# Performance work log

Measured on AMD Instinct MI355X. Metric: run time of the kernel, lower is better.

Reference implementation:

```python
import jax, jax.numpy as jnp
import numpy as np

N, D, HID, G, E2 = 2048, 256, 128, 8, 16384


def _mlp(h, w1, b1, g, be, w2, b2):
    # Linear -> ReLU -> BatchNorm1d (training mode, biased batch var) -> Linear
    h = jax.nn.relu(h @ w1 + b1)
    mu = h.mean(axis=0)
    var = ((h - mu) ** 2).mean(axis=0)
    h = (h - mu) / jnp.sqrt(var + 1e-5) * g + be
    return h @ w2 + b2


def setup_inputs() -> dict:
    key = jax.random.key(0)
    ks = jax.random.split(key, 12)
    x = jax.random.normal(ks[0], (N, D), jnp.float32)
    src = jax.random.randint(ks[1], (E2,), 0, N)
    dst = jax.random.randint(ks[2], (E2,), 0, N)
    src = jnp.where(src == dst, (src + 1) % N, src)  # no self loops
    edge_index = jnp.stack([jnp.concatenate([src, dst]),
                            jnp.concatenate([dst, src])])  # symmetric
    batch = jnp.sort(jax.random.randint(ks[3], (N,), 0, G))
    def lin(k, i, o):
        return 0.1 * jax.random.normal(k, (i, o), jnp.float32)
    out = dict(x=x, edge_index=edge_index, batch=batch)
    dims = [(1, HID, HID), (HID, HID, HID), (HID, HID, 1)]
    names = [("w11", "b11", "g1", "be1", "w12", "b12"),
             ("w21", "b21", "g2", "be2", "w22", "b22"),
             ("w31", "b31", "g3", "be3", "w32", "b32")]
    k = 4
    for (i, h, o), n in zip(dims, names):
        out[n[0]] = lin(ks[k], i, h)
        out[n[1]] = jnp.zeros((h,), jnp.float32)
        out[n[2]] = jnp.ones((h,), jnp.float32)
        out[n[3]] = jnp.zeros((h,), jnp.float32)
        out[n[4]] = lin(ks[k + 1], h, o)
        out[n[5]] = jnp.zeros((o,), jnp.float32)
        k += 2
    return out


def reference(x, edge_index, batch,
              w11, b11, g1, be1, w12, b12,
              w21, b21, g2, be2, w22, b22,
              w31, b31, g3, be3, w32, b32):
    n = x.shape[0]
    # dense adjacency from edge_index; L = D - A (unnormalized graph Laplacian)
    A = jnp.zeros((n, n), x.dtype).at[edge_index[0], edge_index[1]].set(1.0)
    deg = A.sum(axis=1)
    # entropy term: V = x*(Lx) - x*(Ax) + A(x*x), Lx = deg*x - Ax
    Ax = A @ x
    V = x * (deg[:, None] * x - Ax) - x * Ax + A @ (x * x)
    V = jnp.linalg.norm(V, axis=1)  # [n]
    # per-graph softmax over the batch segments
    mx = jax.ops.segment_max(V, batch, num_segments=G)
    ex = jnp.exp(V - mx[batch])
    P = ex / jax.ops.segment_sum(ex, batch, num_segments=G)[batch]
    P = jnp.where(P == 0.0, 1.0, P)
    ent = -P * jnp.log(P)  # [n]

    # GINConv (eps=0): mlp(x + sum_{j in N(i)} x_j) = mlp(x + A @ x)
    def gin(h, w1, b1, g, be, w2, b2):
        return _mlp(h + A @ h, w1, b1, g, be, w2, b2)

    h = gin(ent[:, None], w11, b11, g1, be1, w12, b12)
    h = gin(h, w21, b21, g2, be2, w22, b22)
    h = gin(h, w31, b31, g3, be3, w32, b32)
    p = jax.nn.sigmoid(h[:, 0])  # [n] node probabilities

    gamma = ent.sum()
    loss = gamma - jnp.vdot(ent, p) + jnp.vdot(p, A @ p)

    # greedy conditional expectation (sequential MIS-style selection)
    order = jnp.argsort(-p)

    def step(carry, idx):
        dummy, sel, rej = carry
        nb = A[idx] > 0.0  # neighbor mask [n]
        deg0 = ~jnp.any(nb)
        sel = sel.at[idx].set(sel[idx] | deg0)  # isolated node -> selected
        eligible = (~rej[idx]) & (~sel[idx])
        s = jnp.where(nb, 0.0, dummy).at[idx].set(1.0)
        li = gamma - jnp.vdot(ent, s) + jnp.vdot(s, A @ s)
        accept = eligible & (li <= loss)
        sel = sel.at[idx].set(sel[idx] | accept)
        rej = rej | (nb & accept)
        dummy = jnp.where(accept, s, dummy)
        return (dummy, sel, rej), None

    init = (p, jnp.zeros(n, dtype=bool), jnp.zeros(n, dtype=bool))
    (dummy, sel, rej), _ = jax.lax.scan(step, init, order)

    # graph reconstruction (masked instead of compacted, for static shapes)
    mask = sel.astype(x.dtype)
    x_pooled = x * mask[:, None]
    A2 = A @ A
    A3 = A2 @ A
    eye = jnp.eye(n, dtype=x.dtype)
    adj_pooled = (1.0 - eye) * jnp.clip(A2 + A3, 0.0, 1.0) * (mask[:, None] * mask[None, :])
    batch_pooled = jnp.where(sel, batch, -1)
    return x_pooled, adj_pooled, sel, batch_pooled, loss
```

## Files before the change

### kernel.cpp

```cpp
#include <hip/hip_runtime.h>
#include <math.h>

#define NN 2048
#define DIMF 256
#define HIDN 128
#define NG 8
#define NEDGES 32768
#define W32 32
#define TRI_CAP 131072
#define TRI_LDS 4864

typedef unsigned long long u64;
typedef unsigned char u8;
typedef unsigned short u16;

__global__ void k_init(u64* __restrict__ rowbits, int* __restrict__ segstart) {
  int i = blockIdx.x * blockDim.x + threadIdx.x;
  for (int k = i; k < NN * W32; k += gridDim.x * blockDim.x) rowbits[k] = 0ull;
  if (i <= NG) segstart[i] = NN;
}

__global__ void k_edges(const int* __restrict__ ei, u64* __restrict__ rowbits) {
  int e = blockIdx.x * blockDim.x + threadIdx.x;
  if (e >= NEDGES) return;
  int u = ei[e], v = ei[NEDGES + e];
  atomicOr(&rowbits[((size_t)u << 5) + (v >> 6)], 1ull << (v & 63));
}

__global__ void k_deg(const u64* __restrict__ rowbits, int* __restrict__ deg,
                      const int* __restrict__ batch, int* __restrict__ segstart) {
  int i = blockIdx.x * blockDim.x + threadIdx.x;
  if (i >= NN) return;
  int c = 0;
  for (int w = 0; w < W32; ++w) c += __popcll(rowbits[(i << 5) + w]);
  deg[i] = c;
  if (i == 0 || batch[i] != batch[i - 1]) segstart[batch[i]] = i;
}

__global__ void k_scan2048(const int* __restrict__ in, int* __restrict__ out) {
  __shared__ int part[256];
  int t = threadIdx.x;
  int v[8]; int s = 0;
  for (int k = 0; k < 8; ++k) { v[k] = in[t * 8 + k]; s += v[k]; }
  part[t] = s;
  __syncthreads();
  for (int off = 1; off < 256; off <<= 1) {
    int y = (t >= off) ? part[t - off] : 0;
    __syncthreads();
    part[t] += y;
    __syncthreads();
  }
  int run = part[t] - s;
  for (int k = 0; k < 8; ++k) { out[t * 8 + k] = run; run += v[k]; }
  if (t == 255) out[NN] = part[255];
}

__global__ void k_extract(const u64* __restrict__ rowbits, const int* __restrict__ rp,
                          int* __restrict__ col, int* __restrict__ cnt) {
  int i = blockIdx.x * blockDim.x + threadIdx.x;
  if (i >= NN) return;
  const u64* ri = rowbits + ((size_t)i << 5);
  int o = rp[i];
  for (int w = 0; w < W32; ++w) {
    u64 b = ri[w];
    while (b) { col[o++] = (w << 6) + __builtin_ctzll(b); b &= b - 1; }
  }
  int c = 0;
  for (int e = rp[i]; e < o; ++e) {
    const u64* ra = rowbits + ((size_t)col[e] << 5);
    for (int w = 0; w < W32; ++w) c += __popcll(ra[w] & ri[w]);
  }
  cnt[i] = c;
}

__global__ void k_trifill(const u64* __restrict__ rowbits, const int* __restrict__ rp,
                          const int* __restrict__ col, const int* __restrict__ tp,
                          int2* __restrict__ tri) {
  int i = blockIdx.x * blockDim.x + threadIdx.x;
  if (i >= NN) return;
  const u64* ri = rowbits + ((size_t)i << 5);
  int o = tp[i];
  for (int e = rp[i]; e < rp[i + 1]; ++e) {
    int a = col[e];
    const u64* ra = rowbits + ((size_t)a << 5);
    for (int w = 0; w < W32; ++w) {
      u64 b = ra[w] & ri[w];
      while (b) {
        int j = (w << 6) + __builtin_ctzll(b);
        if (o < TRI_CAP) tri[o] = make_int2(a, j);
        ++o;
        b &= b - 1;
      }
    }
  }
}

__global__ void k_V(const float* __restrict__ x, const int* __restrict__ rp,
                    const int* __restrict__ col, float* __restrict__ V) {
  int i = blockIdx.x; int t = threadIdx.x;
  float xi = x[i * DIMF + t];
  float s1 = 0.f, s2 = 0.f;
  int r0 = rp[i], r1 = rp[i + 1];
  for (int e = r0; e < r1; ++e) {
    float xj = x[col[e] * DIMF + t];
    s1 += xj; s2 += xj * xj;
  }
  float dg = (float)(r1 - r0);
  float val = dg * xi * xi - 2.f * xi * s1 + s2;
  __shared__ double red[DIMF];
  red[t] = (double)val * (double)val;
  __syncthreads();
  for (int off = DIMF / 2; off > 0; off >>= 1) { if (t < off) red[t] += red[t + off]; __syncthreads(); }
  if (t == 0) V[i] = (float)sqrt(red[0]);
}

__global__ void k_soft(const float* __restrict__ V, const int* __restrict__ segstart,
                       float* __restrict__ ent, double* __restrict__ seggamma) {
  int g = blockIdx.x; int t = threadIdx.x;
  int s = segstart[g];
  int e = NN;
  for (int gg = g + 1; gg <= NG; ++gg) { int v = segstart[gg]; if (v < e) e = v; }
  if (s >= e) { if (t == 0) seggamma[g] = 0.0; return; }
  __shared__ float fm[256];
  __shared__ double dd[256];
  float m = -3.0e38f;
  for (int i = s + t; i < e; i += 256) m = fmaxf(m, V[i]);
  fm[t] = m; __syncthreads();
  for (int off = 128; off > 0; off >>= 1) { if (t < off) fm[t] = fmaxf(fm[t], fm[t + off]); __syncthreads(); }
  float mx = fm[0];
  __syncthreads();
  double sum = 0.0;
  for (int i = s + t; i < e; i += 256) sum += exp((double)V[i] - (double)mx);
  dd[t] = sum; __syncthreads();
  for (int off = 128; off > 0; off >>= 1) { if (t < off) dd[t] += dd[t + off]; __syncthreads(); }
  double tot = dd[0];
  __syncthreads();
  double gs = 0.0;
  for (int i = s + t; i < e; i += 256) {
    double P = exp((double)V[i] - (double)mx) / tot;
    float ev = (P > 0.0) ? (float)(-P * log(P)) : 0.f;
    ent[i] = ev;
    gs += (double)ev;
  }
  dd[t] = gs; __syncthreads();
  for (int off = 128; off > 0; off >>= 1) { if (t < off) dd[t] += dd[t + off]; __syncthreads(); }
  if (t == 0) seggamma[g] = dd[0];
}

__global__ void k_agg1(const float* __restrict__ ent, const int* __restrict__ rp,
                       const int* __restrict__ col, float* __restrict__ agg) {
  int i = blockIdx.x * blockDim.x + threadIdx.x;
  if (i >= NN) return;
  float a = ent[i];
  for (int e = rp[i]; e < rp[i + 1]; ++e) a += ent[col[e]];
  agg[i] = a;
}

__global__ void k_lin1(const float* __restrict__ agg, const float* __restrict__ w,
                       const float* __restrict__ b, float* __restrict__ t) {
  int idx = blockIdx.x * blockDim.x + threadIdx.x;
  if (idx >= NN * HIDN) return;
  int i = idx >> 7, k = idx & 127;
  float v = agg[i] * w[k] + b[k];
  t[idx] = v > 0.f ? v : 0.f;
}

__global__ void k_bn(const float* __restrict__ t, const float* __restrict__ g,
                     const float* __restrict__ be, float* __restrict__ scale,
                     float* __restrict__ shift) {
  int k = blockIdx.x; int tid = threadIdx.x;
  __shared__ double red[256];
  double s = 0.0;
  for (int i = tid; i < NN; i += 256) s += (double)t[i * HIDN + k];
  red[tid] = s; __syncthreads();
  for (int off = 128; off > 0; off >>= 1) { if (tid < off) red[tid] += red[tid + off]; __syncthreads(); }
  double mu = red[0] / NN;
  __syncthreads();
  double v = 0.0;
  for (int i = tid; i < NN; i += 256) { double dv = (double)t[i * HIDN + k] - mu; v += dv * dv; }
  red[tid] = v; __syncthreads();
  for (int off = 128; off > 0; off >>= 1) { if (tid < off) red[tid] += red[tid + off]; __syncthreads(); }
  if (tid == 0) {
    float var = (float)(red[0] / NN);
    float sc = g[k] / sqrtf(var + 1e-5f);
    scale[k] = sc;
    shift[k] = be[k] - (float)mu * sc;
  }
}

template<int PRE, int RELU>
__global__ void k_mm(const float* __restrict__ in, const float* __restrict__ Wm,
                     const float* __restrict__ bias, const float* __restrict__ scale,
                     const float* __restrict__ shift, float* __restrict__ out) {
  __shared__ float ti[8][HIDN];
  int r0 = blockIdx.x * 8; int t = threadIdx.x;
  for (int r = 0; r < 8; ++r) {
    float v = in[(r0 + r) * HIDN + t];
    if (PRE) v = v * scale[t] + shift[t];
    ti[r][t] = v;
  }
  __syncthreads();
  float acc[8];
  #pragma unroll
  for (int r = 0; r < 8; ++r) acc[r] = 0.f;
  for (int k = 0; k < HIDN; ++k) {
    float w = Wm[k * HIDN + t];
    #pragma unroll
    for (int r = 0; r < 8; ++r) acc[r] += ti[r][k] * w;
  }
  for (int r = 0; r < 8; ++r) {
    float v = acc[r] + bias[t];
    if (RELU) v = fmaxf(v, 0.f);
    out[(r0 + r) * HIDN + t] = v;
  }
}

__global__ void k_agg128(const float* __restrict__ h, const int* __restrict__ rp,
                         const int* __restrict__ col, float* __restrict__ agg) {
  int i = blockIdx.x; int t = threadIdx.x;
  float a = h[i * HIDN + t];
  for (int e = rp[i]; e < rp[i + 1]; ++e) a += h[col[e] * HIDN + t];
  agg[i * HIDN + t] = a;
}

__global__ void k_lin3(const float* __restrict__ tn, const float* __restrict__ scale,
                       const float* __restrict__ shift, const float* __restrict__ w32,
                       const float* __restrict__ b32, float* __restrict__ p) {
  int i = blockIdx.x; int t = threadIdx.x;
  float v = (tn[i * HIDN + t] * scale[t] + shift[t]) * w32[t];
  __shared__ float red[HIDN];
  red[t] = v; __syncthreads();
  for (int off = 64; off > 0; off >>= 1) { if (t < off) red[t] += red[t + off]; __syncthreads(); }
  if (t == 0) {
    float h3 = red[0] + b32[0];
    p[i] = 1.f / (1.f + expf(-h3));
  }
}

__global__ void k_q0(const float* __restrict__ p, const int* __restrict__ rp,
                     const int* __restrict__ col, float* __restrict__ q0) {
  int i = blockIdx.x * blockDim.x + threadIdx.x;
  if (i >= NN) return;
  float s = 0.f;
  for (int e = rp[i]; e < rp[i + 1]; ++e) s += p[col[e]];
  q0[i] = s;
}

__global__ void k_loss(const float* __restrict__ ent, const float* __restrict__ p,
                       const float* __restrict__ q0, const double* __restrict__ seggamma,
                       double* __restrict__ scal) {
  __shared__ double ra[256], rb[256];
  int t = threadIdx.x;
  double a = 0.0, b = 0.0;
  for (int i = t; i < NN; i += 256) { a += (double)ent[i] * (double)p[i]; b += (double)p[i] * (double)q0[i]; }
  ra[t] = a; rb[t] = b; __syncthreads();
  for (int off = 128; off > 0; off >>= 1) {
    if (t < off) { ra[t] += ra[t + off]; rb[t] += rb[t + off]; }
    __syncthreads();
  }
  if (t == 0) {
    double gamma = 0.0;
    for (int g = 0; g < NG; ++g) gamma += seggamma[g];
    scal[0] = gamma; scal[1] = ra[0]; scal[2] = rb[0];
    scal[3] = gamma - ra[0] + rb[0];
  }
}

__global__ void k_sort(const float* __restrict__ p, int* __restrict__ order) {
  __shared__ u64 s[NN];
  int t = threadIdx.x;
  for (int k = t; k < NN; k += 1024) {
    unsigned b = __float_as_uint(p[k]);
    unsigned ss = (b & 0x80000000u) ? ~b : (b | 0x80000000u);
    s[k] = ((u64)(~ss) << 32) | (unsigned)k;
  }
  __syncthreads();
  for (int k = 2; k <= NN; k <<= 1) {
    for (int j = k >> 1; j > 0; j >>= 1) {
      for (int i = t; i < NN; i += 1024) {
        int ixj = i ^ j;
        if (ixj > i) {
          bool up = ((i & k) == 0);
          u64 a = s[i], b = s[ixj];
          if ((a > b) == up) { s[i] = b; s[ixj] = a; }
        }
      }
      __syncthreads();
    }
  }
  order[t] = (int)(s[t] & 0xFFFFFFFFull);
  order[t + 1024] = (int)(s[t + 1024] & 0xFFFFFFFFull);
}

struct NodeF { float d, q, ent, pad; };

#define DPP4(ctrl)                                                                        \
  a += __int_as_float(__builtin_amdgcn_update_dpp(0, __float_as_int(a), ctrl, 0xf, 0xf, true)); \
  b += __int_as_float(__builtin_amdgcn_update_dpp(0, __float_as_int(b), ctrl, 0xf, 0xf, true)); \
  c += __int_as_float(__builtin_amdgcn_update_dpp(0, __float_as_int(c), ctrl, 0xf, 0xf, true)); \
  d += __int_as_float(__builtin_amdgcn_update_dpp(0, __float_as_int(d), ctrl, 0xf, 0xf, true));

__device__ __forceinline__ void red4(float& a, float& b, float& c, float& d) {
  DPP4(0x111)
  DPP4(0x112)
  DPP4(0x114)
  DPP4(0x118)
  DPP4(0x142)
  DPP4(0x143)
  a = __int_as_float(__builtin_amdgcn_readlane(__float_as_int(a), 63));
  b = __int_as_float(__builtin_amdgcn_readlane(__float_as_int(b), 63));
  c = __int_as_float(__builtin_amdgcn_readlane(__float_as_int(c), 63));
  d = __int_as_float(__builtin_amdgcn_readlane(__float_as_int(d), 63));
}

__global__ void __launch_bounds__(1024, 1) k_greedy(
    const int* __restrict__ rp, const int* __restrict__ col,
    const int* __restrict__ tp, const int2* __restrict__ tri,
    const int* __restrict__ order, const float* __restrict__ p,
    const float* __restrict__ ent, const float* __restrict__ q0,
    const double* __restrict__ scal, u8* __restrict__ selb_g) {
  __shared__ NodeF nd[NN];
  __shared__ u16 colL[NEDGES];
  __shared__ u16 ordl[NN];
  __shared__ unsigned rtL[NN + 2];
  __shared__ ushort2 triL[TRI_LDS];
  __shared__ unsigned decidedL[64], selL[64];
  __shared__ int accf[2][16];
  __shared__ float svS1[2][16], svS2[2][16], svD0[2][16];
  __shared__ double svCr[2][16];
  __shared__ double edL, dAdL;
  int t = threadIdx.x;
  int w = t >> 6, lane = t & 63;

  for (int i = t; i < NN; i += 1024) {
    NodeF v; v.d = p[i]; v.q = q0[i]; v.ent = ent[i]; v.pad = 0.f;
    nd[i] = v;
    ordl[i] = (u16)order[i];
    int tv = tp[i]; if (tv > 65535) tv = 65535;
    rtL[i] = (unsigned)rp[i] | ((unsigned)tv << 16);
  }
  for (int i = t; i < NEDGES; i += 1024) colL[i] = (u16)col[i];
  for (int i = t; i < TRI_LDS; i += 1024) {
    int2 ab = tri[i];
    triL[i] = make_ushort2((u16)(ab.x & 2047), (u16)(ab.y & 2047));
  }
  if (t < 64) { decidedL[t] = 0u; selL[t] = 0u; }
  if (t == 0) {
    int tv = tp[NN]; if (tv > 65535) tv = 65535;
    rtL[NN] = (unsigned)rp[NN] | ((unsigned)tv << 16);
    edL = scal[1]; dAdL = scal[2];
  }
  double gamma = scal[0], loss = scal[3];
  __syncthreads();
  for (int i = t; i < NN; i += 1024) {
    if (((rtL[i + 1] & 0xffffu) - (rtL[i] & 0xffffu)) == 0u) {
      atomicOr(&decidedL[i >> 5], 1u << (i & 31));
      atomicOr(&selL[i >> 5], 1u << (i & 31));
    }
  }
  __syncthreads();

  int pos = 0, rc = 0;
  while (pos < NN) {
    int b = rc & 1; ++rc;
    int accept = 0;
    float S1f = 0.f, S2f = 0.f, d0 = 0.f;
    double crossD = 0.0;
    int step = pos + w;
    if (step < NN) {
      int idx = ordl[step];
      if (!((decidedL[idx >> 5] >> (idx & 31)) & 1u)) {
        unsigned w0 = rtL[idx], w1 = rtL[idx + 1];
        int r0 = w0 & 0xffff, r1 = w1 & 0xffff;
        int t0 = w0 >> 16, t1 = w1 >> 16;
        NodeF vi = nd[idx];
        float s1 = 0.f, s2 = 0.f, sn = 0.f, st = 0.f;
        for (int e = r0 + lane; e < r1; e += 64) {
          int j = colL[e];
          NodeF v = nd[j];
          s1 -= v.ent * v.d; s2 -= v.q * v.d; sn -= v.d;
        }
        if (t1 <= TRI_LDS) {
          for (int e = t0 + lane; e < t1; e += 64) {
            ushort2 ab = triL[e];
            st += nd[ab.x].d * nd[ab.y].d;
          }
        } else {
          int g0 = tp[idx], g1 = tp[idx + 1];
          if (g0 > TRI_CAP) g0 = TRI_CAP;
          if (g1 > TRI_CAP) g1 = TRI_CAP;
          for (int e = g0 + lane; e < g1; e += 64) {
            int2 ab = tri[e];
            st += nd[ab.x].d * nd[ab.y].d;
          }
        }
        red4(s1, s2, sn, st);
        d0 = 1.f - vi.d;
        S1f = s1 + vi.ent * d0;
        S2f = s2 + vi.q * d0;
        crossD = 2.0 * (double)d0 * (double)sn + (double)st;
        double li = gamma - (edL + (double)S1f) + (dAdL + 2.0 * (double)S2f + crossD);
        accept = (li <= loss) ? 1 : 0;
      }
    }
    if (lane == 0) {
      accf[b][w] = accept;
      svS1[b][w] = S1f; svS2[b][w] = S2f; svD0[b][w] = d0; svCr[b][w] = crossD;
    }
    __syncthreads();
    unsigned mask = 0;
    #pragma unroll
    for (int i2 = 0; i2 < 16; ++i2) mask |= (accf[b][i2] ? 1u : 0u) << i2;
    if (mask == 0u) { pos += 16; continue; }
    int k = __builtin_ctz(mask);
    int idx = ordl[pos + k];
    float aS1 = svS1[b][k], aS2 = svS2[b][k], ad0 = svD0[b][k];
    double aCr = svCr[b][k];
    unsigned hw0 = rtL[idx], hw1 = rtL[idx + 1];
    int r0 = hw0 & 0xffff, r1 = hw1 & 0xffff;
    for (int e = r0 + w; e < r1; e += 16) {
      int a = colL[e];
      float da = -nd[a].d;
      if (da != 0.f) {
        unsigned aw0 = rtL[a], aw1 = rtL[a + 1];
        int b0 = aw0 & 0xffff, b1 = aw1 & 0xffff;
        for (int eb = b0 + lane; eb < b1; eb += 64)
          atomicAdd(&nd[colL[eb]].q, da);
      }
    }
    for (int e = r0 + t; e < r1; e += 1024)
      atomicAdd(&nd[colL[e]].q, ad0);
    __syncthreads();
    if (t == 0) {
      nd[idx].d = 1.f;
      atomicOr(&decidedL[idx >> 5], 1u << (idx & 31));
      atomicOr(&selL[idx >> 5], 1u << (idx & 31));
      edL += (double)aS1;
      dAdL += 2.0 * (double)aS2 + aCr;
    }
    for (int e = r0 + t; e < r1; e += 1024) {
      int j = colL[e];
      nd[j].d = 0.f;
      atomicOr(&decidedL[j >> 5], 1u << (j & 31));
    }
    __syncthreads();
    pos += k + 1;
  }
  for (int i = t; i < NN; i += 1024)
    selb_g[i] = (u8)((selL[i >> 5] >> (i & 31)) & 1u);
}

__global__ void k_reach(const u64* __restrict__ src, const int* __restrict__ rp,
                        const int* __restrict__ col, u64* __restrict__ dst) {
  int node = blockIdx.x * 2 + (threadIdx.x >> 5);
  int w = threadIdx.x & 31;
  u64 acc = 0;
  for (int e = rp[node]; e < rp[node + 1]; ++e) acc |= src[((size_t)col[e] << 5) + w];
  dst[((size_t)node << 5) + w] = acc;
}

__global__ void k_out(const u64* __restrict__ row2, const u64* __restrict__ row3,
                      const u8* __restrict__ selb, const float* __restrict__ x,
                      const int* __restrict__ batch, const double* __restrict__ scal,
                      float* __restrict__ o_x, float* __restrict__ o_adj,
                      float* __restrict__ o_sel, float* __restrict__ o_bat,
                      float* __restrict__ o_loss) {
  int idx = blockIdx.x * blockDim.x + threadIdx.x;
  {
    int i = idx >> 11, j = idx & 2047;
    int wo = (i << 5) + (j >> 6);
    u64 b = (row2[wo] | row3[wo]) >> (j & 63);
    o_adj[idx] = ((b & 1ull) && i != j && selb[i] && selb[j]) ? 1.f : 0.f;
  }
  if (idx < NN * DIMF) {
    int i = idx >> 8;
    o_x[idx] = selb[i] ? x[idx] : 0.f;
  }
  if (idx < NN) {
    o_sel[idx] = selb[idx] ? 1.f : 0.f;
    o_bat[idx] = selb[idx] ? (float)batch[idx] : -1.f;
  }
  if (idx == 0) o_loss[0] = (float)scal[3];
}

extern "C" void kernel_launch(void* const* d_in, const int* in_sizes, int n_in,
                              void* d_out, int out_size, void* d_ws, size_t ws_size,
                              hipStream_t stream) {
  const float* x    = (const float*)d_in[0];
  const int*   ei   = (const int*)d_in[1];
  const int*   batch= (const int*)d_in[2];
  const float* w11  = (const float*)d_in[3];
  const float* b11  = (const float*)d_in[4];
  const float* g1   = (const float*)d_in[5];
  const float* be1  = (const float*)d_in[6];
  const float* w12  = (const float*)d_in[7];
  const float* b12  = (const float*)d_in[8];
  const float* w21  = (const float*)d_in[9];
  const float* b21  = (const float*)d_in[10];
  const float* g2   = (const float*)d_in[11];
  const float* be2  = (const float*)d_in[12];
  const float* w22  = (const float*)d_in[13];
  const float* b22  = (const float*)d_in[14];
  const float* w31  = (const float*)d_in[15];
  const float* b31  = (const float*)d_in[16];
  const float* g3   = (const float*)d_in[17];
  const float* be3  = (const float*)d_in[18];
  const float* w32  = (const float*)d_in[19];
  const float* b32  = (const float*)d_in[20];

  char* wsb = (char*)d_ws;
  size_t cur = 0;
  auto alloc = [&](size_t bytes) -> void* {
    void* pp = wsb + cur;
    cur += (bytes + 255) & ~(size_t)255;
    return pp;
  };
  u64*    rowbits = (u64*)alloc((size_t)NN * W32 * 8);
  u64*    row2    = (u64*)alloc((size_t)NN * W32 * 8);
  u64*    row3    = (u64*)alloc((size_t)NN * W32 * 8);
  double* seggam  = (double*)alloc(NG * 8);
  double* scal    = (double*)alloc(4 * 8);
  int*    deg     = (int*)alloc(NN * 4);
  int*    rowptr  = (int*)alloc((NN + 1) * 4);
  int*    colx    = (int*)alloc(65536 * 4);
  int*    tricnt  = (int*)alloc(NN * 4);
  int*    triptr  = (int*)alloc((NN + 1) * 4);
  int2*   tri     = (int2*)alloc((size_t)TRI_CAP * 8);
  int*    segst   = (int*)alloc((NG + 1) * 4);
  int*    order   = (int*)alloc(NN * 4);
  float*  ent     = (float*)alloc(NN * 4);
  float*  V       = (float*)alloc(NN * 4);
  float*  p       = (float*)alloc(NN * 4);
  float*  q0      = (float*)alloc(NN * 4);
  float*  agg1    = (float*)alloc(NN * 4);
  float*  scale   = (float*)alloc(HIDN * 4);
  float*  shift   = (float*)alloc(HIDN * 4);
  float*  tA      = (float*)alloc((size_t)NN * HIDN * 4);
  float*  tB      = (float*)alloc((size_t)NN * HIDN * 4);
  float*  tC      = (float*)alloc((size_t)NN * HIDN * 4);
  u8*     selb    = (u8*)alloc(NN);

  float* out    = (float*)d_out;
  float* o_x    = out;
  float* o_adj  = out + 524288;
  float* o_sel  = out + 4718592;
  float* o_bat  = out + 4720640;
  float* o_loss = out + 4722688;

  k_init<<<64, 256, 0, stream>>>(rowbits, segst);
  k_edges<<<128, 256, 0, stream>>>(ei, rowbits);
  k_deg<<<8, 256, 0, stream>>>(rowbits, deg, batch, segst);
  k_scan2048<<<1, 256, 0, stream>>>(deg, rowptr);
  k_extract<<<8, 256, 0, stream>>>(rowbits, rowptr, colx, tricnt);
  k_scan2048<<<1, 256, 0, stream>>>(tricnt, triptr);
  k_trifill<<<8, 256, 0, stream>>>(rowbits, rowptr, colx, triptr, tri);
  k_V<<<NN, 256, 0, stream>>>(x, rowptr, colx, V);
  k_soft<<<NG, 256, 0, stream>>>(V, segst, ent, seggam);

  k_agg1<<<8, 256, 0, stream>>>(ent, rowptr, colx, agg1);
  k_lin1<<<1024, 256, 0, stream>>>(agg1, w11, b11, tA);
  k_bn<<<HIDN, 256, 0, stream>>>(tA, g1, be1, scale, shift);
  k_mm<1, 0><<<NN / 8, HIDN, 0, stream>>>(tA, w12, b12, scale, shift, tB);
  k_agg128<<<NN, HIDN, 0, stream>>>(tB, rowptr, colx, tC);
  k_mm<0, 1><<<NN / 8, HIDN, 0, stream>>>(tC, w21, b21, scale, shift, tA);
  k_bn<<<HIDN, 256, 0, stream>>>(tA, g2, be2, scale, shift);
  k_mm<1, 0><<<NN / 8, HIDN, 0, stream>>>(tA, w22, b22, scale, shift, tB);
  k_agg128<<<NN, HIDN, 0, stream>>>(tB, rowptr, colx, tC);
  k_mm<0, 1><<<NN / 8, HIDN, 0, stream>>>(tC, w31, b31, scale, shift, tA);
  k_bn<<<HIDN, 256, 0, stream>>>(tA, g3, be3, scale, shift);
  k_lin3<<<NN, HIDN, 0, stream>>>(tA, scale, shift, w32, b32, p);

  k_q0<<<8, 256, 0, stream>>>(p, rowptr, colx, q0);
  k_loss<<<1, 256, 0, stream>>>(ent, p, q0, seggam, scal);
  k_sort<<<1, 1024, 0, stream>>>(p, order);
  k_greedy<<<1, 1024, 0, stream>>>(rowptr, colx, triptr, tri, order, p, ent, q0, scal, selb);

  k_reach<<<NN / 2, 64, 0, stream>>>(rowbits, rowptr, colx, row2);
  k_reach<<<NN / 2, 64, 0, stream>>>(row2, rowptr, colx, row3);
  k_out<<<NN * NN / 256, 256, 0, stream>>>(row2, row3, selb, x, batch, scal,
                                           o_x, o_adj, o_sel, o_bat, o_loss);

  (void)in_sizes; (void)n_in; (void)out_size; (void)ws_size;
}
```

Before: 1.179 ms.

## Maintain neighbor entropy-weighted sums incrementally in greedy MIS to shrink per-candidate work

```diff
diff --git a/kernel.cpp b/kernel.cpp
--- a/kernel.cpp
+++ b/kernel.cpp
@@ -237,13 +237,18 @@
   }
 }
 
-__global__ void k_q0(const float* __restrict__ p, const int* __restrict__ rp,
-                     const int* __restrict__ col, float* __restrict__ q0) {
+__global__ void k_q0(const float* __restrict__ p, const float* __restrict__ ent,
+                     const int* __restrict__ rp, const int* __restrict__ col,
+                     float* __restrict__ q0, float* __restrict__ e0) {
   int i = blockIdx.x * blockDim.x + threadIdx.x;
   if (i >= NN) return;
-  float s = 0.f;
-  for (int e = rp[i]; e < rp[i + 1]; ++e) s += p[col[e]];
-  q0[i] = s;
+  float s = 0.f, es = 0.f;
+  for (int e = rp[i]; e < rp[i + 1]; ++e) {
+    int j = col[e];
+    float pj = p[j];
+    s += pj; es += ent[j] * pj;
+  }
+  q0[i] = s; e0[i] = es;
 }
 
 __global__ void k_loss(const float* __restrict__ ent, const float* __restrict__ p,
@@ -292,25 +297,19 @@
   order[t + 1024] = (int)(s[t + 1024] & 0xFFFFFFFFull);
 }
 
-struct NodeF { float d, q, ent, pad; };
-
-#define DPP4(ctrl)                                                                        \
+#define DPP2(ctrl)                                                                        \
   a += __int_as_float(__builtin_amdgcn_update_dpp(0, __float_as_int(a), ctrl, 0xf, 0xf, true)); \
-  b += __int_as_float(__builtin_amdgcn_update_dpp(0, __float_as_int(b), ctrl, 0xf, 0xf, true)); \
-  c += __int_as_float(__builtin_amdgcn_update_dpp(0, __float_as_int(c), ctrl, 0xf, 0xf, true)); \
-  d += __int_as_float(__builtin_amdgcn_update_dpp(0, __float_as_int(d), ctrl, 0xf, 0xf, true));
-
-__device__ __forceinline__ void red4(float& a, float& b, float& c, float& d) {
-  DPP4(0x111)
-  DPP4(0x112)
-  DPP4(0x114)
-  DPP4(0x118)
-  DPP4(0x142)
-  DPP4(0x143)
+  b += __int_as_float(__builtin_amdgcn_update_dpp(0, __float_as_int(b), ctrl, 0xf, 0xf, true));
+
+__device__ __forceinline__ void red2(float& a, float& b) {
+  DPP2(0x111)
+  DPP2(0x112)
+  DPP2(0x114)
+  DPP2(0x118)
+  DPP2(0x142)
+  DPP2(0x143)
   a = __int_as_float(__builtin_amdgcn_readlane(__float_as_int(a), 63));
   b = __int_as_float(__builtin_amdgcn_readlane(__float_as_int(b), 63));
-  c = __int_as_float(__builtin_amdgcn_readlane(__float_as_int(c), 63));
-  d = __int_as_float(__builtin_amdgcn_readlane(__float_as_int(d), 63));
 }
 
 __global__ void __launch_bounds__(1024, 1) k_greedy(
@@ -318,26 +317,28 @@
     const int* __restrict__ tp, const int2* __restrict__ tri,
     const int* __restrict__ order, const float* __restrict__ p,
     const float* __restrict__ ent, const float* __restrict__ q0,
-    const double* __restrict__ scal, u8* __restrict__ selb_g) {
-  __shared__ NodeF nd[NN];
+    const float* __restrict__ e0, const double* __restrict__ scal,
+    u8* __restrict__ selb_g) {
+  __shared__ float2 dq[NN];
+  __shared__ float2 ee[NN];
   __shared__ u16 colL[NEDGES];
   __shared__ u16 ordl[NN];
-  __shared__ unsigned rtL[NN + 2];
+  __shared__ uint2 rtP[NN + 1];
   __shared__ ushort2 triL[TRI_LDS];
   __shared__ unsigned decidedL[64], selL[64];
-  __shared__ int accf[2][16];
-  __shared__ float svS1[2][16], svS2[2][16], svD0[2][16];
-  __shared__ double svCr[2][16];
-  __shared__ double edL, dAdL;
+  __shared__ unsigned maskL[2];
+  __shared__ float4 svA[2][16];
   int t = threadIdx.x;
   int w = t >> 6, lane = t & 63;
 
   for (int i = t; i < NN; i += 1024) {
-    NodeF v; v.d = p[i]; v.q = q0[i]; v.ent = ent[i]; v.pad = 0.f;
-    nd[i] = v;
+    dq[i] = make_float2(p[i], q0[i]);
+    ee[i] = make_float2(ent[i], e0[i]);
     ordl[i] = (u16)order[i];
-    int tv = tp[i]; if (tv > 65535) tv = 65535;
-    rtL[i] = (unsigned)rp[i] | ((unsigned)tv << 16);
+    int tv0 = tp[i]; if (tv0 > 65535) tv0 = 65535;
+    int tv1 = tp[i + 1]; if (tv1 > 65535) tv1 = 65535;
+    rtP[i] = make_uint2((unsigned)rp[i] | ((unsigned)tv0 << 16),
+                        (unsigned)rp[i + 1] | ((unsigned)tv1 << 16));
   }
   for (int i = t; i < NEDGES; i += 1024) colL[i] = (u16)col[i];
   for (int i = t; i < TRI_LDS; i += 1024) {
@@ -345,15 +346,12 @@
     triL[i] = make_ushort2((u16)(ab.x & 2047), (u16)(ab.y & 2047));
   }
   if (t < 64) { decidedL[t] = 0u; selL[t] = 0u; }
-  if (t == 0) {
-    int tv = tp[NN]; if (tv > 65535) tv = 65535;
-    rtL[NN] = (unsigned)rp[NN] | ((unsigned)tv << 16);
-    edL = scal[1]; dAdL = scal[2];
-  }
+  if (t < 2) maskL[t] = 0u;
   double gamma = scal[0], loss = scal[3];
+  double ed = scal[1], dAd = scal[2];
   __syncthreads();
   for (int i = t; i < NN; i += 1024) {
-    if (((rtL[i + 1] & 0xffffu) - (rtL[i] & 0xffffu)) == 0u) {
+    if (((rtP[i].y & 0xffffu) - (rtP[i].x & 0xffffu)) == 0u) {
       atomicOr(&decidedL[i >> 5], 1u << (i & 31));
       atomicOr(&selL[i >> 5], 1u << (i & 31));
     }
@@ -363,27 +361,24 @@
   int pos = 0, rc = 0;
   while (pos < NN) {
     int b = rc & 1; ++rc;
-    int accept = 0;
-    float S1f = 0.f, S2f = 0.f, d0 = 0.f;
-    double crossD = 0.0;
     int step = pos + w;
     if (step < NN) {
       int idx = ordl[step];
       if (!((decidedL[idx >> 5] >> (idx & 31)) & 1u)) {
-        unsigned w0 = rtL[idx], w1 = rtL[idx + 1];
-        int r0 = w0 & 0xffff, r1 = w1 & 0xffff;
-        int t0 = w0 >> 16, t1 = w1 >> 16;
-        NodeF vi = nd[idx];
-        float s1 = 0.f, s2 = 0.f, sn = 0.f, st = 0.f;
+        uint2 rt = rtP[idx];
+        int r0 = rt.x & 0xffff, r1 = rt.y & 0xffff;
+        int t0 = rt.x >> 16, t1 = rt.y >> 16;
+        float2 dqi = dq[idx];
+        float2 eei = ee[idx];
+        float s2 = 0.f, st = 0.f;
         for (int e = r0 + lane; e < r1; e += 64) {
-          int j = colL[e];
-          NodeF v = nd[j];
-          s1 -= v.ent * v.d; s2 -= v.q * v.d; sn -= v.d;
+          float2 v = dq[colL[e]];
+          s2 -= v.y * v.x;
         }
         if (t1 <= TRI_LDS) {
           for (int e = t0 + lane; e < t1; e += 64) {
             ushort2 ab = triL[e];
-            st += nd[ab.x].d * nd[ab.y].d;
+            st += dq[ab.x].x * dq[ab.y].x;
           }
         } else {
           int g0 = tp[idx], g1 = tp[idx + 1];
@@ -391,56 +386,69 @@
           if (g1 > TRI_CAP) g1 = TRI_CAP;
           for (int e = g0 + lane; e < g1; e += 64) {
             int2 ab = tri[e];
-            st += nd[ab.x].d * nd[ab.y].d;
+            st += dq[ab.x].x * dq[ab.y].x;
           }
         }
-        red4(s1, s2, sn, st);
-        d0 = 1.f - vi.d;
-        S1f = s1 + vi.ent * d0;
-        S2f = s2 + vi.q * d0;
-        crossD = 2.0 * (double)d0 * (double)sn + (double)st;
-        double li = gamma - (edL + (double)S1f) + (dAdL + 2.0 * (double)S2f + crossD);
-        accept = (li <= loss) ? 1 : 0;
+        red2(s2, st);
+        float d0 = 1.f - dqi.x;
+        float S1 = -eei.y + eei.x * d0;
+        float S2 = s2 + dqi.y * d0;
+        float sn = -dqi.y;
+        double cross = 2.0 * (double)d0 * (double)sn + (double)st;
+        double li = gamma - (ed + (double)S1) + (dAd + 2.0 * (double)S2 + cross);
+        if (li <= loss && lane == 0) {
+          svA[b][w] = make_float4(S1, S2, d0, st);
+          atomicOr(&maskL[b], 1u << w);
+        }
       }
     }
-    if (lane == 0) {
-      accf[b][w] = accept;
-      svS1[b][w] = S1f; svS2[b][w] = S2f; svD0[b][w] = d0; svCr[b][w] = crossD;
-    }
-    __syncthreads();
-    unsigned mask = 0;
-    #pragma unroll
-    for (int i2 = 0; i2 < 16; ++i2) mask |= (accf[b][i2] ? 1u : 0u) << i2;
+    __syncthreads();
+    unsigned mask = maskL[b];
     if (mask == 0u) { pos += 16; continue; }
     int k = __builtin_ctz(mask);
     int idx = ordl[pos + k];
-    float aS1 = svS1[b][k], aS2 = svS2[b][k], ad0 = svD0[b][k];
-    double aCr = svCr[b][k];
-    unsigned hw0 = rtL[idx], hw1 = rtL[idx + 1];
-    int r0 = hw0 & 0xffff, r1 = hw1 & 0xffff;
+    float4 A = svA[b][k];
+    float2 dqi = dq[idx];
+    uint2 rt = rtP[idx];
+    int r0 = rt.x & 0xffff, r1 = rt.y & 0xffff;
+    {
+      double cross = 2.0 * (double)A.z * (double)(-dqi.y) + (double)A.w;
+      ed += (double)A.x;
+      dAd += 2.0 * (double)A.y + cross;
+    }
+    __syncthreads();
+    if (t == 0) maskL[b] = 0u;
     for (int e = r0 + w; e < r1; e += 16) {
       int a = colL[e];
-      float da = -nd[a].d;
+      float da = -dq[a].x;
       if (da != 0.f) {
-        unsigned aw0 = rtL[a], aw1 = rtL[a + 1];
-        int b0 = aw0 & 0xffff, b1 = aw1 & 0xffff;
-        for (int eb = b0 + lane; eb < b1; eb += 64)
-          atomicAdd(&nd[colL[eb]].q, da);
+        float ea = ee[a].x;
+        uint2 art = rtP[a];
+        int b0 = art.x & 0xffff, b1 = art.y & 0xffff;
+        for (int eb = b0 + lane; eb < b1; eb += 64) {
+          int bb = colL[eb];
+          atomicAdd(&dq[bb].y, da);
+          atomicAdd(&ee[bb].y, ea * da);
+        }
       }
     }
-    for (int e = r0 + t; e < r1; e += 1024)
-      atomicAdd(&nd[colL[e]].q, ad0);
+    {
+      float ei = ee[idx].x;
+      for (int e = r0 + t; e < r1; e += 1024) {
+        int bb = colL[e];
+        atomicAdd(&dq[bb].y, A.z);
+        atomicAdd(&ee[bb].y, ei * A.z);
+      }
+    }
     __syncthreads();
     if (t == 0) {
-      nd[idx].d = 1.f;
+      dq[idx].x = 1.f;
       atomicOr(&decidedL[idx >> 5], 1u << (idx & 31));
       atomicOr(&selL[idx >> 5], 1u << (idx & 31));
-      edL += (double)aS1;
-      dAdL += 2.0 * (double)aS2 + aCr;
     }
     for (int e = r0 + t; e < r1; e += 1024) {
       int j = colL[e];
-      nd[j].d = 0.f;
+      dq[j].x = 0.f;
       atomicOr(&decidedL[j >> 5], 1u << (j & 31));
     }
     __syncthreads();
@@ -532,6 +540,7 @@
   float*  V       = (float*)alloc(NN * 4);
   float*  p       = (float*)alloc(NN * 4);
   float*  q0      = (float*)alloc(NN * 4);
+  float*  e0      = (float*)alloc(NN * 4);
   float*  agg1    = (float*)alloc(NN * 4);
   float*  scale   = (float*)alloc(HIDN * 4);
   float*  shift   = (float*)alloc(HIDN * 4);
@@ -570,10 +579,10 @@
   k_bn<<<HIDN, 256, 0, stream>>>(tA, g3, be3, scale, shift);
   k_lin3<<<NN, HIDN, 0, stream>>>(tA, scale, shift, w32, b32, p);
 
-  k_q0<<<8, 256, 0, stream>>>(p, rowptr, colx, q0);
+  k_q0<<<8, 256, 0, stream>>>(p, ent, rowptr, colx, q0, e0);
   k_loss<<<1, 256, 0, stream>>>(ent, p, q0, seggam, scal);
   k_sort<<<1, 1024, 0, stream>>>(p, order);
-  k_greedy<<<1, 1024, 0, stream>>>(rowptr, colx, triptr, tri, order, p, ent, q0, scal, selb);
+  k_greedy<<<1, 1024, 0, stream>>>(rowptr, colx, triptr, tri, order, p, ent, q0, e0, scal, selb);
 
   k_reach<<<NN / 2, 64, 0, stream>>>(rowbits, rowptr, colx, row2);
   k_reach<<<NN / 2, 64, 0, stream>>>(row2, rowptr, colx, row3);
```

After: 1.132 ms. 1.04x faster.
